# Kernel tuning notes

Measured on AMD Instinct MI355X. Metric: run time of the kernel, lower is better.

Reference implementation:

```python
import jax, jax.numpy as jnp
import numpy as np
from jax import lax

T, H, D = 2048, 64, 64  # seq_length, num_heads, head_size


def setup_inputs() -> dict:
    key = jax.random.key(0)
    ks = jax.random.split(key, 7)
    r = jax.random.normal(ks[0], (T, H * D), jnp.float32)
    # decay exponents must be negative so exp(w) in (e^-1, 1); otherwise the
    # length-T product of per-step decays overflows (faithful math, stable data)
    w = -jax.random.uniform(ks[1], (T, H * D), dtype=jnp.float32)
    k = jax.random.normal(ks[2], (T, H * D), jnp.float32)
    v = jax.random.normal(ks[3], (T, H * D), jnp.float32)
    # a/b form a low-rank state correction; scale down to keep the linear
    # recurrence spectrally stable over T steps (as normalized kk does in RWKV-7)
    a = jax.random.normal(ks[4], (T, H * D), jnp.float32) * 0.1
    b = jax.random.normal(ks[5], (T, H * D), jnp.float32) * 0.1
    state2 = jnp.zeros((H, D, D), jnp.float32)
    return {"seq_length": T, "r": r, "w": w, "k": k, "v": v, "a": a, "b": b,
            "state2": state2}


def _wkv7_scan(r, w, k, v, a, b, state2, seq_length):
    Hh, Dd = state2.shape[0], state2.shape[1]
    rs = r.reshape(seq_length, Hh, Dd)
    ws = w.reshape(seq_length, Hh, Dd)
    ks_ = k.reshape(seq_length, Hh, Dd)
    vs = v.reshape(seq_length, Hh, Dd)
    as_ = a.reshape(seq_length, Hh, Dd)
    bs = b.reshape(seq_length, Hh, Dd)

    def step(s, inp):
        r_t, w_t, k_t, v_t, a_t, b_t = inp
        # s: [H, D, D]; per-head: s = s*exp(w) + (s@a)@b + v@k  (a col, k/b rows)
        sa = jnp.einsum('hij,hj->hi', s, a_t)                      # s @ a -> [H, D]
        s = (s * jnp.exp(w_t)[:, None, :]
             + sa[:, :, None] * b_t[:, None, :]
             + v_t[:, :, None] * k_t[:, None, :])
        x_t = jnp.einsum('hij,hj->hi', s, r_t)                     # s @ r -> [H, D]
        return s, x_t

    state2_out, xs = lax.scan(step, state2, (rs, ws, ks_, vs, as_, bs))
    x = xs[:, :, None, :]  # [T, H, 1, D] as in the torch module's final view
    return x, state2_out


def reference(seq_length, r, w, k, v, a, b, state2):
    return _wkv7_scan(r, w, k, v, a, b, state2, seq_length)
```

## Files before the change

kernel.cpp:

```cpp
#include <hip/hip_runtime.h>


typedef float f32x4 __attribute__((ext_vector_type(4)));

constexpr int T_LEN = 2048;
constexpr int DD    = 64;
constexpr int HD    = 64 * 64;

#define AS1 __attribute__((address_space(1)))
#define AS3 __attribute__((address_space(3)))

struct Buf { f32x4 r, e, k, a, b; float vv; };

__global__ __launch_bounds__(256)
void exp_kernel(const float4* __restrict__ w, float4* __restrict__ ew, int n4) {
  int i = blockIdx.x * blockDim.x + threadIdx.x;
  int stride = gridDim.x * blockDim.x;
  for (; i < n4; i += stride) {
    float4 x = w[i];
    float4 o;
    o.x = __expf(x.x); o.y = __expf(x.y); o.z = __expf(x.z); o.w = __expf(x.w);
    ew[i] = o;
  }
}

template<int CTRL>
__device__ __forceinline__ float dpp_add(float x) {
  int y = __builtin_amdgcn_update_dpp(0, __float_as_int(x), CTRL, 0xf, 0xf, true);
  return x + __int_as_float(y);
}

__device__ __forceinline__ float row16_reduce(float x) {
  x = dpp_add<0xB1>(x);
  x = dpp_add<0x4E>(x);
  x = dpp_add<0x141>(x);
  x = dpp_add<0x140>(x);
  return x;
}

__device__ __forceinline__ void duo_reduce(float& a, float& b) {
  float t0, t1;
  asm volatile(
    "s_nop 1\n\t"
    "v_mov_b32_dpp %2, %0 quad_perm:[1,0,3,2] row_mask:0xf bank_mask:0xf\n\t"
    "v_mov_b32_dpp %3, %1 quad_perm:[1,0,3,2] row_mask:0xf bank_mask:0xf\n\t"
    "s_nop 0\n\t"
    "v_add_f32 %0, %0, %2\n\t"
    "v_add_f32 %1, %1, %3\n\t"
    "s_nop 0\n\t"
    "v_mov_b32_dpp %2, %0 quad_perm:[2,3,0,1] row_mask:0xf bank_mask:0xf\n\t"
    "v_mov_b32_dpp %3, %1 quad_perm:[2,3,0,1] row_mask:0xf bank_mask:0xf\n\t"
    "s_nop 0\n\t"
    "v_add_f32 %0, %0, %2\n\t"
    "v_add_f32 %1, %1, %3\n\t"
    "s_nop 0\n\t"
    "v_mov_b32_dpp %2, %0 row_half_mirror row_mask:0xf bank_mask:0xf\n\t"
    "v_mov_b32_dpp %3, %1 row_half_mirror row_mask:0xf bank_mask:0xf\n\t"
    "s_nop 0\n\t"
    "v_add_f32 %0, %0, %2\n\t"
    "v_add_f32 %1, %1, %3\n\t"
    "s_nop 0\n\t"
    "v_mov_b32_dpp %2, %0 row_mirror row_mask:0xf bank_mask:0xf\n\t"
    "v_mov_b32_dpp %3, %1 row_mirror row_mask:0xf bank_mask:0xf\n\t"
    "s_nop 0\n\t"
    "v_add_f32 %0, %0, %2\n\t"
    "v_add_f32 %1, %1, %3"
    : "+v"(a), "+v"(b), "=&v"(t0), "=&v"(t1));
}

__device__ __forceinline__ float dot4(const f32x4& x, const f32x4& y) {
  return fmaf(x[3], y[3], fmaf(x[2], y[2], fmaf(x[1], y[1], x[0] * y[0])));
}

__device__ __forceinline__ void gload_lds16(const float* g, const float* l) {
  __builtin_amdgcn_global_load_lds((const AS1 unsigned*)g, (AS3 unsigned*)l, 16, 0, 0);
}

__global__ __launch_bounds__(64, 1)
void wkv7_scan(const float* __restrict__ R, const float* __restrict__ EW,
               const float* __restrict__ K, const float* __restrict__ V,
               const float* __restrict__ A, const float* __restrict__ B,
               const float* __restrict__ S0, float* __restrict__ X,
               float* __restrict__ SOUT)
{
  __shared__ float smem[4096];

  const int blk = blockIdx.x;
  const int xcd = blk & 7;
  const int m   = blk >> 3;
  const int h   = xcd * 8 + (m & 7);
  const int br  = m >> 3;

  const int lane = threadIdx.x;
  const int cg   = lane & 15;
  const int rl   = lane >> 4;
  const int row  = br * 4 + rl;
  const int c0   = cg * 4;

  const int g1  = lane >> 4;
  const int sub = lane & 15;
  const float* base1 = (g1 == 0) ? R : (g1 == 1) ? EW : (g1 == 2) ? K : A;
  const float* base2 = (g1 == 0) ? B : V;
  const float* p1 = base1 + h * DD + sub * 4;
  const float* p2 = base2 + h * DD + sub * 4;

  const unsigned lb  = (unsigned)(uintptr_t)(AS3 float*)&smem[0];
  const unsigned vab = lb + (unsigned)(cg * 16);
  const unsigned vvb = lb + (unsigned)(row * 4);

  const int voffb = (h * DD + row) * 4;

  f32x4 s;
  {
    const f32x4* sp = (const f32x4*)(S0 + (size_t)h * DD * DD + row * DD + c0);
    s = *sp;
  }

  auto stage = [&](int tt, int slot) {
    const size_t o = (size_t)tt * HD;
    const float* l = &smem[slot * 512];
    gload_lds16(p1 + o, l);
    gload_lds16(p2 + o, l + 256);
  };

  auto lds_read = [&](Buf& d, int slot) {
    unsigned va = vab + (unsigned)(slot * 2048);
    unsigned vv = vvb + (unsigned)(slot * 2048);
    asm volatile(
      "ds_read_b128 %0, %6\n\t"
      "ds_read_b128 %1, %6 offset:256\n\t"
      "ds_read_b128 %2, %6 offset:512\n\t"
      "ds_read_b128 %3, %6 offset:768\n\t"
      "ds_read_b128 %4, %6 offset:1024\n\t"
      "ds_read_b32  %5, %7 offset:1280"
      : "=&v"(d.r), "=&v"(d.e), "=&v"(d.k), "=&v"(d.a), "=&v"(d.b), "=&v"(d.vv)
      : "v"(va), "v"(vv) : "memory");
  };

  auto wait_nx1 = [&](Buf& d) {
    asm volatile("s_waitcnt lgkmcnt(6)"
                 : "+v"(d.r), "+v"(d.e), "+v"(d.k), "+v"(d.a), "+v"(d.b),
                   "+v"(d.vv));
  };

  float sa;
  float yprev = 0.0f;
  int   yoff_prev = 2047 * (HD * 4) + voffb;

  auto body = [&](Buf& cur, Buf& nx1, Buf& nx2, int t) {
    asm volatile("s_waitcnt vmcnt(15)" ::: "memory");
    lds_read(nx2, (t + 2) & 7);
    wait_nx1(nx1);

    const float vv = cur.vv;
    s[0] = fmaf(cur.e[0], s[0], fmaf(sa, cur.b[0], vv * cur.k[0]));
    s[1] = fmaf(cur.e[1], s[1], fmaf(sa, cur.b[1], vv * cur.k[1]));
    s[2] = fmaf(cur.e[2], s[2], fmaf(sa, cur.b[2], vv * cur.k[2]));
    s[3] = fmaf(cur.e[3], s[3], fmaf(sa, cur.b[3], vv * cur.k[3]));

    float qd = dot4(s, nx1.a);
    float yd = dot4(s, cur.r);

    if (cg == 0) {
      asm volatile("global_store_dword %0, %1, %2"
                   :: "v"(yoff_prev), "v"(yprev), "s"(X) : "memory");
    }
    stage((t + 8) & (T_LEN - 1), t & 7);

    duo_reduce(qd, yd);
    sa    = qd;
    yprev = yd;
    yoff_prev = t * (HD * 4) + voffb;
  };

  for (int i = 0; i < 8; ++i) {
    stage(i, i);
    __builtin_amdgcn_sched_barrier(0);
  }
  asm volatile("s_waitcnt vmcnt(12)" ::: "memory");

  Buf B0, B1, B2, B3;
  lds_read(B0, 0);
  lds_read(B1, 1);
  asm volatile("s_waitcnt lgkmcnt(0)"
               : "+v"(B0.r), "+v"(B0.e), "+v"(B0.k), "+v"(B0.a), "+v"(B0.b),
                 "+v"(B0.vv), "+v"(B1.a));

  sa = row16_reduce(dot4(s, B0.a));

  for (int t = 0; t < T_LEN; t += 4) {
    body(B0, B1, B2, t);
    body(B1, B2, B3, t + 1);
    body(B2, B3, B0, t + 2);
    body(B3, B0, B1, t + 3);
  }

  if (cg == 0) {
    asm volatile("global_store_dword %0, %1, %2"
                 :: "v"(yoff_prev), "v"(yprev), "s"(X) : "memory");
  }

  *(f32x4*)(SOUT + (size_t)h * DD * DD + row * DD + c0) = s;
}

extern "C" void kernel_launch(void* const* d_in, const int* in_sizes, int n_in,
                              void* d_out, int out_size, void* d_ws, size_t ws_size,
                              hipStream_t stream) {
  const float* r  = (const float*)d_in[1];
  const float* w  = (const float*)d_in[2];
  const float* k  = (const float*)d_in[3];
  const float* v  = (const float*)d_in[4];
  const float* a  = (const float*)d_in[5];
  const float* b  = (const float*)d_in[6];
  const float* s0 = (const float*)d_in[7];

  float* x    = (float*)d_out;
  float* sout = x + (size_t)T_LEN * HD;

  float* ew = (float*)d_ws;
  (void)ws_size; (void)in_sizes; (void)n_in;

  int n4 = T_LEN * HD / 4;
  hipLaunchKernelGGL(exp_kernel, dim3(1024), dim3(256), 0, stream,
                     (const float4*)w, (float4*)ew, n4);
  hipLaunchKernelGGL(wkv7_scan, dim3(1024), dim3(64), 0, stream,
                     r, ew, k, v, a, b, s0, x, sout);
}
```

Measured before the change: 291.0 us.

## Give each lane eight state columns and halve the scan grid

Each lane now holds 8 state elements (two float4 vectors) instead of 4, so a row spans 8 lanes and each wave covers 8 rows. The grid shrinks from 1024 to 512 waves. The cross-lane DPP reduction drops from 4 stages to 3, which shortens the serial per-timestep dependency chain, and the redundant per-head input staging is halved. In exchange each lane does longer dot products and more LDS reads per step, and there are fewer waves to hide latency.

```diff
diff --git a/kernel.cpp b/kernel.cpp
--- a/kernel.cpp
+++ b/kernel.cpp
@@ -10,7 +10,7 @@
 #define AS1 __attribute__((address_space(1)))
 #define AS3 __attribute__((address_space(3)))
 
-struct Buf { f32x4 r, e, k, a, b; float vv; };
+struct Buf { f32x4 r0, r1, e0, e1, k0, k1, a0, a1, b0, b1; float vv; };
 
 __global__ __launch_bounds__(256)
 void exp_kernel(const float4* __restrict__ w, float4* __restrict__ ew, int n4) {
@@ -30,15 +30,14 @@
   return x + __int_as_float(y);
 }
 
-__device__ __forceinline__ float row16_reduce(float x) {
+__device__ __forceinline__ float row8_reduce(float x) {
   x = dpp_add<0xB1>(x);
   x = dpp_add<0x4E>(x);
   x = dpp_add<0x141>(x);
-  x = dpp_add<0x140>(x);
   return x;
 }
 
-__device__ __forceinline__ void duo_reduce(float& a, float& b) {
+__device__ __forceinline__ void duo_reduce8(float& a, float& b) {
   float t0, t1;
   asm volatile(
     "s_nop 1\n\t"
@@ -56,12 +55,6 @@
     "s_nop 0\n\t"
     "v_mov_b32_dpp %2, %0 row_half_mirror row_mask:0xf bank_mask:0xf\n\t"
     "v_mov_b32_dpp %3, %1 row_half_mirror row_mask:0xf bank_mask:0xf\n\t"
-    "s_nop 0\n\t"
-    "v_add_f32 %0, %0, %2\n\t"
-    "v_add_f32 %1, %1, %3\n\t"
-    "s_nop 0\n\t"
-    "v_mov_b32_dpp %2, %0 row_mirror row_mask:0xf bank_mask:0xf\n\t"
-    "v_mov_b32_dpp %3, %1 row_mirror row_mask:0xf bank_mask:0xf\n\t"
     "s_nop 0\n\t"
     "v_add_f32 %0, %0, %2\n\t"
     "v_add_f32 %1, %1, %3"
@@ -92,28 +85,28 @@
   const int br  = m >> 3;
 
   const int lane = threadIdx.x;
-  const int cg   = lane & 15;
-  const int rl   = lane >> 4;
-  const int row  = br * 4 + rl;
-  const int c0   = cg * 4;
-
-  const int g1  = lane >> 4;
-  const int sub = lane & 15;
+  const int cg   = lane & 7;
+  const int rl   = lane >> 3;
+  const int row  = br * 8 + rl;
+  const int c0   = cg * 8;
+
+  const int g1    = lane >> 4;
+  const int sub16 = lane & 15;
   const float* base1 = (g1 == 0) ? R : (g1 == 1) ? EW : (g1 == 2) ? K : A;
   const float* base2 = (g1 == 0) ? B : V;
-  const float* p1 = base1 + h * DD + sub * 4;
-  const float* p2 = base2 + h * DD + sub * 4;
+  const float* p1 = base1 + h * DD + sub16 * 4;
+  const float* p2 = base2 + h * DD + sub16 * 4;
 
   const unsigned lb  = (unsigned)(uintptr_t)(AS3 float*)&smem[0];
-  const unsigned vab = lb + (unsigned)(cg * 16);
+  const unsigned vab = lb + (unsigned)(cg * 32);
   const unsigned vvb = lb + (unsigned)(row * 4);
 
   const int voffb = (h * DD + row) * 4;
 
-  f32x4 s;
+  f32x4 s0, s1;
   {
     const f32x4* sp = (const f32x4*)(S0 + (size_t)h * DD * DD + row * DD + c0);
-    s = *sp;
+    s0 = sp[0]; s1 = sp[1];
   }
 
   auto stage = [&](int tt, int slot) {
@@ -127,20 +120,28 @@
     unsigned va = vab + (unsigned)(slot * 2048);
     unsigned vv = vvb + (unsigned)(slot * 2048);
     asm volatile(
-      "ds_read_b128 %0, %6\n\t"
-      "ds_read_b128 %1, %6 offset:256\n\t"
-      "ds_read_b128 %2, %6 offset:512\n\t"
-      "ds_read_b128 %3, %6 offset:768\n\t"
-      "ds_read_b128 %4, %6 offset:1024\n\t"
-      "ds_read_b32  %5, %7 offset:1280"
-      : "=&v"(d.r), "=&v"(d.e), "=&v"(d.k), "=&v"(d.a), "=&v"(d.b), "=&v"(d.vv)
+      "ds_read_b128 %0, %11\n\t"
+      "ds_read_b128 %1, %11 offset:16\n\t"
+      "ds_read_b128 %2, %11 offset:256\n\t"
+      "ds_read_b128 %3, %11 offset:272\n\t"
+      "ds_read_b128 %4, %11 offset:512\n\t"
+      "ds_read_b128 %5, %11 offset:528\n\t"
+      "ds_read_b128 %6, %11 offset:768\n\t"
+      "ds_read_b128 %7, %11 offset:784\n\t"
+      "ds_read_b128 %8, %11 offset:1024\n\t"
+      "ds_read_b128 %9, %11 offset:1040\n\t"
+      "ds_read_b32  %10, %12 offset:1280"
+      : "=&v"(d.r0), "=&v"(d.r1), "=&v"(d.e0), "=&v"(d.e1),
+        "=&v"(d.k0), "=&v"(d.k1), "=&v"(d.a0), "=&v"(d.a1),
+        "=&v"(d.b0), "=&v"(d.b1), "=&v"(d.vv)
       : "v"(va), "v"(vv) : "memory");
   };
 
   auto wait_nx1 = [&](Buf& d) {
-    asm volatile("s_waitcnt lgkmcnt(6)"
-                 : "+v"(d.r), "+v"(d.e), "+v"(d.k), "+v"(d.a), "+v"(d.b),
-                   "+v"(d.vv));
+    asm volatile("s_waitcnt lgkmcnt(11)"
+                 : "+v"(d.r0), "+v"(d.r1), "+v"(d.e0), "+v"(d.e1),
+                   "+v"(d.k0), "+v"(d.k1), "+v"(d.a0), "+v"(d.a1),
+                   "+v"(d.b0), "+v"(d.b1), "+v"(d.vv));
   };
 
   float sa;
@@ -153,13 +154,17 @@
     wait_nx1(nx1);
 
     const float vv = cur.vv;
-    s[0] = fmaf(cur.e[0], s[0], fmaf(sa, cur.b[0], vv * cur.k[0]));
-    s[1] = fmaf(cur.e[1], s[1], fmaf(sa, cur.b[1], vv * cur.k[1]));
-    s[2] = fmaf(cur.e[2], s[2], fmaf(sa, cur.b[2], vv * cur.k[2]));
-    s[3] = fmaf(cur.e[3], s[3], fmaf(sa, cur.b[3], vv * cur.k[3]));
-
-    float qd = dot4(s, nx1.a);
-    float yd = dot4(s, cur.r);
+    s0[0] = fmaf(cur.e0[0], s0[0], fmaf(sa, cur.b0[0], vv * cur.k0[0]));
+    s0[1] = fmaf(cur.e0[1], s0[1], fmaf(sa, cur.b0[1], vv * cur.k0[1]));
+    s0[2] = fmaf(cur.e0[2], s0[2], fmaf(sa, cur.b0[2], vv * cur.k0[2]));
+    s0[3] = fmaf(cur.e0[3], s0[3], fmaf(sa, cur.b0[3], vv * cur.k0[3]));
+    s1[0] = fmaf(cur.e1[0], s1[0], fmaf(sa, cur.b1[0], vv * cur.k1[0]));
+    s1[1] = fmaf(cur.e1[1], s1[1], fmaf(sa, cur.b1[1], vv * cur.k1[1]));
+    s1[2] = fmaf(cur.e1[2], s1[2], fmaf(sa, cur.b1[2], vv * cur.k1[2]));
+    s1[3] = fmaf(cur.e1[3], s1[3], fmaf(sa, cur.b1[3], vv * cur.k1[3]));
+
+    float qd = dot4(s0, nx1.a0) + dot4(s1, nx1.a1);
+    float yd = dot4(s0, cur.r0) + dot4(s1, cur.r1);
 
     if (cg == 0) {
       asm volatile("global_store_dword %0, %1, %2"
@@ -167,7 +172,7 @@
     }
     stage((t + 8) & (T_LEN - 1), t & 7);
 
-    duo_reduce(qd, yd);
+    duo_reduce8(qd, yd);
     sa    = qd;
     yprev = yd;
     yoff_prev = t * (HD * 4) + voffb;
@@ -183,10 +188,11 @@
   lds_read(B0, 0);
   lds_read(B1, 1);
   asm volatile("s_waitcnt lgkmcnt(0)"
-               : "+v"(B0.r), "+v"(B0.e), "+v"(B0.k), "+v"(B0.a), "+v"(B0.b),
-                 "+v"(B0.vv), "+v"(B1.a));
-
-  sa = row16_reduce(dot4(s, B0.a));
+               : "+v"(B0.r0), "+v"(B0.e0), "+v"(B0.k0), "+v"(B0.a0),
+                 "+v"(B0.b0), "+v"(B0.a1), "+v"(B0.vv), "+v"(B1.a0),
+                 "+v"(B1.a1));
+
+  sa = row8_reduce(dot4(s0, B0.a0) + dot4(s1, B0.a1));
 
   for (int t = 0; t < T_LEN; t += 4) {
     body(B0, B1, B2, t);
@@ -200,7 +206,8 @@
                  :: "v"(yoff_prev), "v"(yprev), "s"(X) : "memory");
   }
 
-  *(f32x4*)(SOUT + (size_t)h * DD * DD + row * DD + c0) = s;
+  f32x4* so = (f32x4*)(SOUT + (size_t)h * DD * DD + row * DD + c0);
+  so[0] = s0; so[1] = s1;
 }
 
 extern "C" void kernel_launch(void* const* d_in, const int* in_sizes, int n_in,
@@ -223,6 +230,6 @@
   int n4 = T_LEN * HD / 4;
   hipLaunchKernelGGL(exp_kernel, dim3(1024), dim3(256), 0, stream,
                      (const float4*)w, (float4*)ew, n4);
-  hipLaunchKernelGGL(wkv7_scan, dim3(1024), dim3(64), 0, stream,
+  hipLaunchKernelGGL(wkv7_scan, dim3(512), dim3(64), 0, stream,
                      r, ew, k, v, a, b, s0, x, sout);
 }
```

After: 437.7 us. 1.5x slower.
